# Performance work log

Hardware: AMD Instinct MI355X
Metric: run time of the kernel (lower is better)

## Reference

```python
import jax, jax.numpy as jnp
import numpy as np

WEIGHTS = (0.5, 1.0, 2.0)   # per-channel weights (init kwarg)
INVERTED = True             # init kwarg


def setup_inputs() -> dict:
    key = jax.random.key(0)
    B, C, H, W = 16, 3, 256, 256
    # binary flood mask: nonzero = foreground (scipy EDT measures distance to nearest zero)
    flood = jax.random.randint(key, (B, C, H, W), 0, 2).astype(jnp.float32)
    return {"flood_batch": flood}


def _edt_squared(mask):
    """Exact squared Euclidean distance transform per [H,W] slice.

    mask: bool [B,C,H,W], True = foreground (nonzero). Returns float32 [B,C,H,W]
    squared distance from each True pixel to the nearest False pixel (0 at False).
    Uses the exact separable decomposition:
      D2[r,w] = min_{r'} ( g[r',w]^2 + (r-r')^2 ),  g = 1D horizontal distance to zero.
    """
    B, C, H, W = mask.shape
    BIG = jnp.float32(H + W)  # exceeds any achievable 1D distance

    # --- pass 1: 1D distance to nearest zero along W (forward + backward scans) ---
    m = jnp.moveaxis(mask, -1, 0)  # [W,B,C,H]

    def step(carry, mm):
        d = jnp.where(mm, jnp.minimum(carry + 1.0, BIG), 0.0)
        return d, d

    init = jnp.full((B, C, H), BIG, jnp.float32)
    _, fwd = jax.lax.scan(step, init, m)
    _, bwd = jax.lax.scan(step, init, m[::-1])
    g = jnp.minimum(fwd, bwd[::-1])          # [W,B,C,H]
    g2 = jnp.moveaxis(g, 0, -1) ** 2          # [B,C,H,W]

    # --- pass 2: exact min-plus over rows (vectorized over B,C,W; scan over output row) ---
    rows = jnp.arange(H, dtype=jnp.float32)

    def row_step(_, r):
        cand = g2 + ((r - rows) ** 2)[None, None, :, None]  # [B,C,H,W]
        return None, cand.min(axis=2)                        # [B,C,W]

    _, d2 = jax.lax.scan(row_step, None, rows)  # [H,B,C,W]
    return jnp.moveaxis(d2, 0, 2)               # [B,C,H,W]


def reference(flood_batch):
    w = jnp.asarray(WEIGHTS, jnp.float32)
    dt = jnp.sqrt(_edt_squared(flood_batch != 0))            # [B,C,H,W]
    dt = dt * w[None, :, None, None]                         # per-channel weight
    mx = dt.max(axis=(2, 3), keepdims=True)                  # per-slice max
    safe = jnp.where(mx > 0, mx, 1.0)
    scaled = (mx - dt) / safe if INVERTED else dt / safe
    return jnp.where(mx > 0, scaled, dt)
```

## Files before the change

### kernel.cpp

```cpp
#include <hip/hip_runtime.h>


#define PADV 1e30f

__global__ __launch_bounds__(256) void k1_g16(const float* __restrict__ in,
                                              unsigned short* __restrict__ g) {
    int row = blockIdx.x * 4 + (threadIdx.x >> 6);
    int lane = threadIdx.x & 63;
    const float4 m = ((const float4*)in)[(long)row * 64 + lane];

    unsigned long long b[4];
    b[0] = __ballot(m.x == 0.f);
    b[1] = __ballot(m.y == 0.f);
    b[2] = __ballot(m.z == 0.f);
    b[3] = __ballot(m.w == 0.f);

    unsigned long long loP = ~0ull >> (63 - lane);
    unsigned long long loM = loP >> 1;
    unsigned long long hiP = ~0ull << lane;
    unsigned long long hiM = hiP << 1;

    int LP[4], LM[4], RP[4], RM[4];
    #pragma unroll
    for (int cc = 0; cc < 4; ++cc) {
        unsigned long long mlp = b[cc] & loP;
        unsigned long long mlm = b[cc] & loM;
        unsigned long long mhp = b[cc] & hiP;
        unsigned long long mhm = b[cc] & hiM;
        LP[cc] = mlp ? 4 * (63 - __builtin_clzll(mlp)) + cc : -1000;
        LM[cc] = mlm ? 4 * (63 - __builtin_clzll(mlm)) + cc : -1000;
        RP[cc] = mhp ? 4 * __builtin_ctzll(mhp) + cc : 2000;
        RM[cc] = mhm ? 4 * __builtin_ctzll(mhm) + cc : 2000;
    }
    int qp1 = max(LP[0], LP[1]);
    int qp2 = max(qp1, LP[2]);
    int qp3 = max(qp2, LP[3]);
    int sm3 = LM[3];
    int sm2 = max(LM[2], sm3);
    int sm1 = max(LM[1], sm2);
    int colL0 = max(LP[0], sm1);
    int colL1 = max(qp1, sm2);
    int colL2 = max(qp2, sm3);
    int colL3 = qp3;
    int sp2 = min(RP[2], RP[3]);
    int sp1 = min(RP[1], sp2);
    int sp0 = min(RP[0], sp1);
    int pm0 = RM[0];
    int pm1 = min(pm0, RM[1]);
    int pm2 = min(pm1, RM[2]);
    int colR0 = sp0;
    int colR1 = min(pm0, sp1);
    int colR2 = min(pm1, sp2);
    int colR3 = min(pm2, RP[3]);

    int p0 = lane * 4;
    int d0 = min(min(p0 - colL0, colR0 - p0), 512);
    int d1 = min(min(p0 + 1 - colL1, colR1 - p0 - 1), 512);
    int d2 = min(min(p0 + 2 - colL2, colR2 - p0 - 2), 512);
    int d3 = min(min(p0 + 3 - colL3, colR3 - p0 - 3), 512);

    ushort4 v;
    v.x = (unsigned short)d0; v.y = (unsigned short)d1;
    v.z = (unsigned short)d2; v.w = (unsigned short)d3;
    ((ushort4*)(g + (long)row * 256))[lane] = v;
}

__global__ __launch_bounds__(256) __attribute__((amdgpu_waves_per_eu(4)))
void k2_colpass(const unsigned short* __restrict__ g,
                float* __restrict__ d2out,
                float* __restrict__ stripmax) {
    __shared__ float tile[16 * 161];
    __shared__ float wm[4];
    int bx = blockIdx.x;
    int slice = bx >> 5;
    int sub = bx & 31;
    int strip = sub >> 1;
    int half = sub & 1;
    int w0 = strip * 16;
    int base = half * 128;
    int tid = threadIdx.x;

    if (tid < 160) {
        int r = base - 16 + tid;
        if (r >= 0 && r < 256) {
            const uint4* src = (const uint4*)(g + (long)slice * 65536 + (long)r * 256 + w0);
            #pragma unroll
            for (int j = 0; j < 2; ++j) {
                uint4 q = src[j];
                unsigned vv[4] = {q.x, q.y, q.z, q.w};
                #pragma unroll
                for (int e = 0; e < 4; ++e) {
                    float dl = (float)(vv[e] & 0xffffu);
                    float dh = (float)(vv[e] >> 16);
                    int col = j * 8 + e * 2;
                    tile[col * 161 + tid] = dl * dl;
                    tile[(col + 1) * 161 + tid] = dh * dh;
                }
            }
        } else {
            #pragma unroll
            for (int cc = 0; cc < 16; ++cc) tile[cc * 161 + tid] = PADV;
        }
    }
    __syncthreads();

    int c = tid & 15;
    int rg = tid >> 4;
    int i0 = 16 + rg * 8;
    float own[8], lo[16], hi[16];
    #pragma unroll
    for (int k = 0; k < 8; ++k) own[k] = tile[c * 161 + i0 + k];
    #pragma unroll
    for (int i = 0; i < 16; ++i) {
        lo[i] = tile[c * 161 + i0 - 16 + i];
        hi[i] = tile[c * 161 + i0 + 8 + i];
    }

    float dmin[8];
    #pragma unroll
    for (int k = 0; k < 8; ++k) dmin[k] = own[k];
    #pragma unroll
    for (int o = 1; o <= 16; ++o) {
        float oo = (float)(o * o);
        #pragma unroll
        for (int k = 0; k < 8; ++k) {
            int jm = k - o, jp = k + o;
            float a = (jm >= 0) ? own[jm] : lo[jm + 16];
            float b = (jp < 8) ? own[jp] : hi[jp - 8];
            dmin[k] = fminf(dmin[k], fminf(a, b) + oo);
        }
    }

    int p = w0 + c;
    int r0 = base + rg * 8;
    #pragma unroll
    for (int k = 0; k < 8; ++k) {
        if (dmin[k] > 288.0f) {
            float best = dmin[k];
            int r = r0 + k;
            const unsigned short* col = g + (long)slice * 65536 + p;
            for (int rp = 0; rp < 256; ++rp) {
                float gv = (float)col[rp * 256];
                float dr = (float)(r - rp);
                best = fminf(best, fmaf(dr, dr, gv * gv));
            }
            dmin[k] = best;
        }
    }

    float* dst = d2out + (long)slice * 65536 + w0 + c;
    float mmax = 0.f;
    #pragma unroll
    for (int k = 0; k < 8; ++k) {
        dst[(long)(r0 + k) * 256] = dmin[k];
        mmax = fmaxf(mmax, dmin[k]);
    }
    #pragma unroll
    for (int off = 32; off >= 1; off >>= 1)
        mmax = fmaxf(mmax, __shfl_down(mmax, off, 64));
    if ((tid & 63) == 0) wm[tid >> 6] = mmax;
    __syncthreads();
    if (tid == 0)
        stripmax[bx] = fmaxf(fmaxf(wm[0], wm[1]), fmaxf(wm[2], wm[3]));
}

__global__ __launch_bounds__(256) void k3_final(float* __restrict__ out,
                                                const float* __restrict__ stripmax) {
    __shared__ float sMx;
    int tid = threadIdx.x;
    int idx4 = blockIdx.x * 256 + tid;
    int slice = blockIdx.x >> 6;
    if (tid < 32) {
        float v = stripmax[slice * 32 + tid];
        #pragma unroll
        for (int off = 16; off >= 1; off >>= 1) v = fmaxf(v, __shfl_down(v, off, 64));
        if (tid == 0) sMx = v;
    }
    __syncthreads();

    int c = slice % 3;
    float wgt = (c == 0) ? 0.5f : ((c == 1) ? 1.0f : 2.0f);
    float mx = wgt * __builtin_sqrtf(sMx);

    float4 d2 = ((float4*)out)[idx4];
    float4 r;
    if (mx > 0.f) {
        float inv = 1.0f / mx;
        r.x = (mx - wgt * __builtin_sqrtf(d2.x)) * inv;
        r.y = (mx - wgt * __builtin_sqrtf(d2.y)) * inv;
        r.z = (mx - wgt * __builtin_sqrtf(d2.z)) * inv;
        r.w = (mx - wgt * __builtin_sqrtf(d2.w)) * inv;
    } else {
        r.x = wgt * __builtin_sqrtf(d2.x);
        r.y = wgt * __builtin_sqrtf(d2.y);
        r.z = wgt * __builtin_sqrtf(d2.z);
        r.w = wgt * __builtin_sqrtf(d2.w);
    }
    ((float4*)out)[idx4] = r;
}

extern "C" void kernel_launch(void* const* d_in, const int* in_sizes, int n_in,
                              void* d_out, int out_size, void* d_ws, size_t ws_size,
                              hipStream_t stream) {
    const float* in = (const float*)d_in[0];
    float* out = (float*)d_out;
    float* stripmax = (float*)d_ws;
    unsigned short* g = (unsigned short*)((char*)d_ws + 8192);

    k1_g16<<<3072, 256, 0, stream>>>(in, g);
    k2_colpass<<<1536, 256, 0, stream>>>(g, out, stripmax);
    k3_final<<<3072, 256, 0, stream>>>(out, stripmax);
}
```

Baseline: 80.30 us.

## Split column pass into quarter-height blocks and double k3 work per thread

The column min-plus kernel now splits each 16-column strip into four 64-row chunks instead of two 128-row chunks. That doubles the block count to 3072, halves the rows per thread to 4, and has two threads load each tile row. The aim is more parallelism and lower register pressure, at the cost of a larger halo overhead (96 loaded rows for 64 outputs instead of 160 for 128). The final normalisation kernel now handles two float4 per thread with half as many blocks, and reduces 64 strip maxima per slice. The workspace offset for g moves to make room for the larger stripmax array.

```diff
diff --git a/kernel.cpp b/kernel.cpp
--- a/kernel.cpp
+++ b/kernel.cpp
@@ -69,72 +69,71 @@
 void k2_colpass(const unsigned short* __restrict__ g,
                 float* __restrict__ d2out,
                 float* __restrict__ stripmax) {
-    __shared__ float tile[16 * 161];
+    __shared__ float tile[16 * 101];
     __shared__ float wm[4];
     int bx = blockIdx.x;
-    int slice = bx >> 5;
-    int sub = bx & 31;
-    int strip = sub >> 1;
-    int half = sub & 1;
+    int slice = bx >> 6;
+    int sub = bx & 63;
+    int strip = sub >> 2;
+    int quarter = sub & 3;
     int w0 = strip * 16;
-    int base = half * 128;
+    int base = quarter * 64;
     int tid = threadIdx.x;
 
-    if (tid < 160) {
-        int r = base - 16 + tid;
+    if (tid < 192) {
+        int idx = tid >> 1;
+        int half = tid & 1;
+        int colbase = half * 8;
+        int r = base - 16 + idx;
         if (r >= 0 && r < 256) {
-            const uint4* src = (const uint4*)(g + (long)slice * 65536 + (long)r * 256 + w0);
+            uint4 q = *(const uint4*)(g + (long)slice * 65536 + (long)r * 256 + w0 + colbase);
+            unsigned vv[4] = {q.x, q.y, q.z, q.w};
             #pragma unroll
-            for (int j = 0; j < 2; ++j) {
-                uint4 q = src[j];
-                unsigned vv[4] = {q.x, q.y, q.z, q.w};
-                #pragma unroll
-                for (int e = 0; e < 4; ++e) {
-                    float dl = (float)(vv[e] & 0xffffu);
-                    float dh = (float)(vv[e] >> 16);
-                    int col = j * 8 + e * 2;
-                    tile[col * 161 + tid] = dl * dl;
-                    tile[(col + 1) * 161 + tid] = dh * dh;
-                }
+            for (int e = 0; e < 4; ++e) {
+                float dl = (float)(vv[e] & 0xffffu);
+                float dh = (float)(vv[e] >> 16);
+                tile[(colbase + 2 * e) * 101 + idx] = dl * dl;
+                tile[(colbase + 2 * e + 1) * 101 + idx] = dh * dh;
             }
         } else {
             #pragma unroll
-            for (int cc = 0; cc < 16; ++cc) tile[cc * 161 + tid] = PADV;
+            for (int e = 0; e < 8; ++e) tile[(colbase + e) * 101 + idx] = PADV;
         }
     }
     __syncthreads();
 
     int c = tid & 15;
     int rg = tid >> 4;
-    int i0 = 16 + rg * 8;
-    float own[8], lo[16], hi[16];
-    #pragma unroll
-    for (int k = 0; k < 8; ++k) own[k] = tile[c * 161 + i0 + k];
+    int i0 = 16 + rg * 4;
+
+    float own[4], lo[16], hi[16];
+    #pragma unroll
+    for (int k = 0; k < 4; ++k) own[k] = tile[c * 101 + i0 + k];
     #pragma unroll
     for (int i = 0; i < 16; ++i) {
-        lo[i] = tile[c * 161 + i0 - 16 + i];
-        hi[i] = tile[c * 161 + i0 + 8 + i];
-    }
-
-    float dmin[8];
-    #pragma unroll
-    for (int k = 0; k < 8; ++k) dmin[k] = own[k];
+        lo[i] = tile[c * 101 + i0 - 16 + i];
+        hi[i] = tile[c * 101 + i0 + 4 + i];
+    }
+
+    float dmin[4];
+    #pragma unroll
+    for (int k = 0; k < 4; ++k) dmin[k] = own[k];
     #pragma unroll
     for (int o = 1; o <= 16; ++o) {
         float oo = (float)(o * o);
         #pragma unroll
-        for (int k = 0; k < 8; ++k) {
+        for (int k = 0; k < 4; ++k) {
             int jm = k - o, jp = k + o;
             float a = (jm >= 0) ? own[jm] : lo[jm + 16];
-            float b = (jp < 8) ? own[jp] : hi[jp - 8];
+            float b = (jp < 4) ? own[jp] : hi[jp - 4];
             dmin[k] = fminf(dmin[k], fminf(a, b) + oo);
         }
     }
 
     int p = w0 + c;
-    int r0 = base + rg * 8;
-    #pragma unroll
-    for (int k = 0; k < 8; ++k) {
+    int r0 = base + rg * 4;
+    #pragma unroll
+    for (int k = 0; k < 4; ++k) {
         if (dmin[k] > 288.0f) {
             float best = dmin[k];
             int r = r0 + k;
@@ -151,7 +150,7 @@
     float* dst = d2out + (long)slice * 65536 + w0 + c;
     float mmax = 0.f;
     #pragma unroll
-    for (int k = 0; k < 8; ++k) {
+    for (int k = 0; k < 4; ++k) {
         dst[(long)(r0 + k) * 256] = dmin[k];
         mmax = fmaxf(mmax, dmin[k]);
     }
@@ -168,35 +167,40 @@
                                                 const float* __restrict__ stripmax) {
     __shared__ float sMx;
     int tid = threadIdx.x;
-    int idx4 = blockIdx.x * 256 + tid;
-    int slice = blockIdx.x >> 6;
-    if (tid < 32) {
-        float v = stripmax[slice * 32 + tid];
+    int slice = blockIdx.x >> 5;
+    if (tid < 64) {
+        float v = stripmax[slice * 64 + tid];
         #pragma unroll
-        for (int off = 16; off >= 1; off >>= 1) v = fmaxf(v, __shfl_down(v, off, 64));
+        for (int off = 32; off >= 1; off >>= 1) v = fmaxf(v, __shfl_down(v, off, 64));
         if (tid == 0) sMx = v;
     }
     __syncthreads();
 
-    int c = slice % 3;
-    float wgt = (c == 0) ? 0.5f : ((c == 1) ? 1.0f : 2.0f);
+    int ch = slice % 3;
+    float wgt = (ch == 0) ? 0.5f : ((ch == 1) ? 1.0f : 2.0f);
     float mx = wgt * __builtin_sqrtf(sMx);
 
-    float4 d2 = ((float4*)out)[idx4];
-    float4 r;
-    if (mx > 0.f) {
-        float inv = 1.0f / mx;
-        r.x = (mx - wgt * __builtin_sqrtf(d2.x)) * inv;
-        r.y = (mx - wgt * __builtin_sqrtf(d2.y)) * inv;
-        r.z = (mx - wgt * __builtin_sqrtf(d2.z)) * inv;
-        r.w = (mx - wgt * __builtin_sqrtf(d2.w)) * inv;
-    } else {
-        r.x = wgt * __builtin_sqrtf(d2.x);
-        r.y = wgt * __builtin_sqrtf(d2.y);
-        r.z = wgt * __builtin_sqrtf(d2.z);
-        r.w = wgt * __builtin_sqrtf(d2.w);
-    }
-    ((float4*)out)[idx4] = r;
+    int idx4 = blockIdx.x * 512 + tid;
+    float4* o4 = (float4*)out;
+    #pragma unroll
+    for (int rep = 0; rep < 2; ++rep) {
+        int i4 = idx4 + rep * 256;
+        float4 d2 = o4[i4];
+        float4 r;
+        if (mx > 0.f) {
+            float inv = 1.0f / mx;
+            r.x = (mx - wgt * __builtin_sqrtf(d2.x)) * inv;
+            r.y = (mx - wgt * __builtin_sqrtf(d2.y)) * inv;
+            r.z = (mx - wgt * __builtin_sqrtf(d2.z)) * inv;
+            r.w = (mx - wgt * __builtin_sqrtf(d2.w)) * inv;
+        } else {
+            r.x = wgt * __builtin_sqrtf(d2.x);
+            r.y = wgt * __builtin_sqrtf(d2.y);
+            r.z = wgt * __builtin_sqrtf(d2.z);
+            r.w = wgt * __builtin_sqrtf(d2.w);
+        }
+        o4[i4] = r;
+    }
 }
 
 extern "C" void kernel_launch(void* const* d_in, const int* in_sizes, int n_in,
@@ -205,9 +209,9 @@
     const float* in = (const float*)d_in[0];
     float* out = (float*)d_out;
     float* stripmax = (float*)d_ws;
-    unsigned short* g = (unsigned short*)((char*)d_ws + 8192);
+    unsigned short* g = (unsigned short*)((char*)d_ws + 16384);
 
     k1_g16<<<3072, 256, 0, stream>>>(in, g);
-    k2_colpass<<<1536, 256, 0, stream>>>(g, out, stripmax);
-    k3_final<<<3072, 256, 0, stream>>>(out, stripmax);
-}
+    k2_colpass<<<3072, 256, 0, stream>>>(g, out, stripmax);
+    k3_final<<<1536, 256, 0, stream>>>(out, stripmax);
+}
```

Measured after the change: 81.73 us. No clear change (+1.8%).
